# Performance work log

Hardware: AMD Instinct MI355X
Metric: run time of the kernel (lower is better)

The kernel has to match this reference:

```python
import jax, jax.numpy as jnp
import numpy as np

B, S, E, H = 16, 2048, 128, 128  # batch, seq_len, n_embd, head_dim


def setup_inputs() -> dict:
    key = jax.random.key(0)
    ks = jax.random.split(key, 6)
    init_s = 1.0 / np.sqrt(E)  # ~ torch Linear default init scale
    return {
        "q": jax.random.normal(ks[0], (B, S, E), jnp.float32),
        "k": jax.random.normal(ks[1], (B, S, E), jnp.float32),
        "v": jax.random.normal(ks[2], (B, S, E), jnp.float32),
        "Wq": jax.random.normal(ks[3], (H, E), jnp.float32) * init_s,
        "bq": jnp.zeros((H,), jnp.float32),
        "Wk": jax.random.normal(ks[4], (H, E), jnp.float32) * init_s,
        "bk": jnp.zeros((H,), jnp.float32),
        "Wv": jax.random.normal(ks[5], (H, E), jnp.float32) * init_s,
        "bv": jnp.zeros((H,), jnp.float32),
        "mask": jnp.tril(jnp.ones((S, S), jnp.float32)),  # causal mask
    }


def reference(q, k, v, Wq, bq, Wk, bk, Wv, bv, mask):
    # Linear projections: y = x @ W.T + b (torch nn.Linear convention)
    qh = q @ Wq.T + bq  # [B,S,H]
    kh = k @ Wk.T + bk  # [B,S,H]
    vh = v @ Wv.T + bv  # [B,S,H]
    d_k = kh.shape[-1]
    wei = jnp.einsum("bqd,bkd->bqk", qh, kh) * (d_k ** -0.5)  # [B,S,S]
    wei = jnp.where(mask == 0, -jnp.inf, wei)  # masked_fill(mask==0, -inf)
    attn = jax.nn.softmax(wei, axis=-1)
    return jnp.einsum("bqk,bkd->bqd", attn, vh)  # [B,S,H]
```

## Files before the change

### kernel.cpp

```cpp
#include <hip/hip_runtime.h>
#include <hip/hip_bf16.h>

#define BATCH 16
#define SEQ   2048
#define HD    128
#define TB    64
#define QB3   64
#define KB3   64
#define NT3   (SEQ/QB3)
#define PLANE ((size_t)BATCH*SEQ*HD)

typedef __attribute__((ext_vector_type(8))) short bf16x8;
typedef __attribute__((ext_vector_type(4))) float f32x4;
typedef __attribute__((ext_vector_type(2))) unsigned int u32x2;

#define MFMA(a,b,c) __builtin_amdgcn_mfma_f32_16x16x32_bf16(a,b,c,0,0,0)

__device__ __forceinline__ short f2bf(float f){
  union{float f; unsigned u;} v; v.f = f;
  unsigned r = (v.u + 0x7FFFu + ((v.u>>16)&1u))>>16;
  return (short)r;
}
__device__ __forceinline__ unsigned packbf(float lo, float hi){
  return ((unsigned)(unsigned short)f2bf(hi) << 16) | (unsigned short)f2bf(lo);
}
__device__ __forceinline__ bf16x8 pack8(f32x4 a, f32x4 b){
  bf16x8 r;
  r[0]=f2bf(a[0]); r[1]=f2bf(a[1]); r[2]=f2bf(a[2]); r[3]=f2bf(a[3]);
  r[4]=f2bf(b[0]); r[5]=f2bf(b[1]); r[6]=f2bf(b[2]); r[7]=f2bf(b[3]);
  return r;
}
__device__ __forceinline__ bf16x8 ldfrag(const float* base, size_t eo){
  const float* p = base + eo;
  return pack8(*(const f32x4*)p, *(const f32x4*)(p+4));
}

__global__ __launch_bounds__(256)
void wconv_kernel(const float* __restrict__ Wq, const float* __restrict__ Wk,
                  const float* __restrict__ Wv, short* __restrict__ wb)
{
  int i = (blockIdx.x*256 + threadIdx.x)*8;
  const float* src = (i < 16384) ? Wq : (i < 32768 ? Wk : Wv);
  int off = i & 16383;
  f32x4 a = *(const f32x4*)(src + off);
  f32x4 b = *(const f32x4*)(src + off + 4);
  *(bf16x8*)(wb + i) = pack8(a, b);
}

__global__ __launch_bounds__(256)
void proj_kernel(const float* __restrict__ q, const float* __restrict__ k,
                 const float* __restrict__ v,
                 const float* __restrict__ bq, const float* __restrict__ bk,
                 const float* __restrict__ bv,
                 const short* __restrict__ wb, short* __restrict__ ws)
{
  __shared__ __align__(16) short T[TB*136];
  __shared__ __align__(16) short VT[HD*72];

  const int z = blockIdx.y;
  const float* x  = z==0 ? q  : (z==1 ? k  : v);
  const float* bb = z==0 ? bq : (z==1 ? bk : bv);
  const short* W  = wb + (size_t)z*HD*HD;

  const int tid = threadIdx.x;
  const int w = tid>>6, l = tid&63, li = l&15, g = l>>4;
  const int bx = blockIdx.x;
  const int rowbase = bx*TB + w*16;

  bf16x8 afr[4];
  const float* xr = x + (size_t)(rowbase+li)*HD + g*8;
  #pragma unroll
  for (int ks=0; ks<4; ks++) afr[ks] = ldfrag(xr, (size_t)ks*32);

  f32x4 acc[8];
  #pragma unroll
  for (int ct=0; ct<8; ct++) acc[ct] = (f32x4){0.f,0.f,0.f,0.f};
  #pragma unroll
  for (int ct=0; ct<8; ct++){
    #pragma unroll
    for (int ks=0; ks<4; ks++){
      bf16x8 bfr = *(const bf16x8*)(W + (size_t)(ct*16+li)*HD + ks*32 + g*8);
      acc[ct] = MFMA(afr[ks], bfr, acc[ct]);
    }
  }

  const int img  = (bx>>1);
  const int half = bx & 1;

  if (z < 2){
    #pragma unroll
    for (int ct=0; ct<8; ct++){
      float bias = bb[ct*16+li];
      #pragma unroll
      for (int r=0; r<4; r++)
        T[(w*16+g*4+r)*136 + ct*16+li] = f2bf(acc[ct][r] + bias);
    }
    __syncthreads();
    if (z == 0){
      short* dst = ws + (size_t)bx*TB*HD;
      #pragma unroll
      for (int it=0; it<4; it++){
        int c = tid + it*256, row = c>>4, c8 = c&15;
        *(bf16x8*)(dst + row*HD + c8*8) = *(const bf16x8*)&T[row*136 + c8*8];
      }
    } else {
      short* dst = ws + PLANE + (size_t)img*16384;
      #pragma unroll
      for (int it=0; it<4; it++){
        int c = tid + it*256, row = c>>4, c8 = c&15;
        int r128 = half*64 + row;
        int chunk = r128*16 + (c8 ^ (r128&7));
        *(bf16x8*)(dst + chunk*8) = *(const bf16x8*)&T[row*136 + c8*8];
      }
    }
  } else {
    #pragma unroll
    for (int ct=0; ct<8; ct++){
      float bias = bb[ct*16+li];
      #pragma unroll
      for (int r=0; r<4; r++)
        VT[(ct*16+li)*72 + w*16+g*4+r] = f2bf(acc[ct][r] + bias);
    }
    __syncthreads();
    short* dst = ws + 2*PLANE + (size_t)img*16384;
    const int d = tid>>1, hf = tid&1;
    #pragma unroll
    for (int j=0; j<4; j++){
      int c8l = hf*4 + j;
      int c8g = half*8 + c8l;
      int chunk = d*16 + (c8g ^ (d&7));
      *(bf16x8*)(dst + chunk*8) = *(const bf16x8*)&VT[d*72 + c8l*8];
    }
  }
}

__global__ __launch_bounds__(256, 2)
void attn_kernel(const short* __restrict__ ws, float* __restrict__ out)
{
  __shared__ __align__(16) short KVL[2][16384];
  __shared__ __align__(16) short PL[4][16*72];

  const int bid  = blockIdx.x;
  const int xcd  = bid & 7, slot = bid >> 3;
  const int b    = xcd*2 + (slot >> 5);
  const int sl   = slot & 31;
  const int qt   = (slot < 32) ? sl : (31 - sl);

  const int tid = threadIdx.x;
  const int w = tid>>6, l = tid&63, li = l&15, g = l>>4;

  const short* Qw    = ws;
  const short* KimgB = ws + PLANE   + (size_t)b*(SEQ/128)*16384;
  const short* VimgB = ws + 2*PLANE + (size_t)b*(SEQ/128)*16384;

  const size_t qbase = (size_t)b*SEQ + qt*QB3;
  short* Pw = &PL[w][0];
  const float sc = 0.088388347648318447f;

  bf16x8 qfr[4];
  #pragma unroll
  for (int ks=0; ks<4; ks++)
    qfr[ks] = *(const bf16x8*)&Qw[(qbase + w*16 + li)*HD + ks*32 + g*8];

  f32x4 oacc[8];
  #pragma unroll
  for (int dt=0; dt<8; dt++) oacc[dt] = (f32x4){0.f,0.f,0.f,0.f};
  float mreg = -1e30f, lreg = 0.f;

  bf16x8 stg[8];
  #define LOADT(kt_) do{                                                     \
    const short* sK = KimgB + (size_t)((kt_)>>1)*16384 + ((kt_)&1)*8192;     \
    const short* sV = VimgB + (size_t)((kt_)>>1)*16384;                      \
    const int vh = ((kt_)&1)*8;                                              \
    _Pragma("unroll")                                                        \
    for (int j=0;j<4;j++) stg[j] = *(const bf16x8*)(sK + (tid + j*256)*8);   \
    _Pragma("unroll")                                                        \
    for (int j=0;j<4;j++){                                                   \
      int i = tid + j*256, d = i>>3, c8s = i&7;                              \
      stg[4+j] = *(const bf16x8*)(sV + (d*16 + vh + c8s)*8);                 \
    }                                                                        \
  }while(0)
  #define WRT(nb_) do{                                                      \
    short* dK = &KVL[nb_][0];                                               \
    short* dV = &KVL[nb_][8192];                                            \
    _Pragma("unroll")                                                       \
    for (int j=0;j<4;j++) *(bf16x8*)(dK + (tid+j*256)*8) = stg[j];          \
    _Pragma("unroll")                                                       \
    for (int j=0;j<4;j++) *(bf16x8*)(dV + (tid+j*256)*8) = stg[4+j];        \
  }while(0)

  LOADT(0); WRT(0); __syncthreads();
  int cur = 0;

  for (int kt=0; kt<=qt; kt++){
    const bool pre = (kt < qt);
    if (pre) LOADT(kt+1);

    const short* KL = &KVL[cur][0];
    const short* VL = &KVL[cur][8192];

    f32x4 st[4];
    #pragma unroll
    for (int ct=0; ct<4; ct++) st[ct] = (f32x4){0.f,0.f,0.f,0.f};
    __builtin_amdgcn_s_setprio(1);
    #pragma unroll
    for (int ct=0; ct<4; ct++){
      const int row = ct*16 + li;
      #pragma unroll
      for (int ks=0; ks<4; ks++){
        const int chunk = row*16 + ((ks*4 + g) ^ (row&7));
        bf16x8 kfr = *(const bf16x8*)&KL[chunk*8];
        st[ct] = MFMA(kfr, qfr[ks], st[ct]);
      }
    }
    __builtin_amdgcn_s_setprio(0);

    float sv[4][4];
    float pm = -1e30f;
    const bool diag = (kt == qt);
    const int qloc = w*16 + li;
    #pragma unroll
    for (int ct=0; ct<4; ct++){
      #pragma unroll
      for (int r=0; r<4; r++){
        float x = st[ct][r]*sc;
        if (diag && (ct*16 + g*4 + r) > qloc) x = -1e30f;
        sv[ct][r] = x;
        pm = fmaxf(pm, x);
      }
    }
    pm = fmaxf(pm, __shfl_xor(pm, 16));
    pm = fmaxf(pm, __shfl_xor(pm, 32));
    float mn   = fmaxf(mreg, pm);
    float sclq = __expf(mreg - mn);
    mreg = mn;
    float psum = 0.f;
    #pragma unroll
    for (int ct=0; ct<4; ct++){
      #pragma unroll
      for (int r=0; r<4; r++){
        float p = __expf(sv[ct][r] - mn);
        sv[ct][r] = p;
        psum += p;
      }
    }
    psum += __shfl_xor(psum, 16);
    psum += __shfl_xor(psum, 32);
    lreg = lreg*sclq + psum;

    float sclo[4];
    #pragma unroll
    for (int r=0; r<4; r++) sclo[r] = __shfl(sclq, g*4 + r);
    #pragma unroll
    for (int dt=0; dt<8; dt++){
      #pragma unroll
      for (int r=0; r<4; r++) oacc[dt][r] *= sclo[r];
    }

    #pragma unroll
    for (int c4=0; c4<4; c4++){
      u32x2 pw;
      pw[0] = packbf(sv[c4][0], sv[c4][1]);
      pw[1] = packbf(sv[c4][2], sv[c4][3]);
      *(u32x2*)&Pw[li*72 + c4*16 + g*4] = pw;
    }
    __builtin_amdgcn_s_setprio(1);
    #pragma unroll
    for (int ks2=0; ks2<2; ks2++){
      bf16x8 afr = *(const bf16x8*)&Pw[li*72 + ks2*32 + g*8];
      #pragma unroll
      for (int dt=0; dt<8; dt++){
        const int d = dt*16 + li;
        const int chunk = d*8 + ((ks2*4 + g) ^ (d&7));
        bf16x8 bfr = *(const bf16x8*)&VL[chunk*8];
        oacc[dt] = MFMA(afr, bfr, oacc[dt]);
      }
    }
    __builtin_amdgcn_s_setprio(0);

    if (pre) WRT(cur^1);
    __syncthreads();
    cur ^= 1;
  }

  float lso[4];
  #pragma unroll
  for (int r=0; r<4; r++) lso[r] = __shfl(lreg, g*4 + r);
  float* Ob = out + qbase*HD;
  #pragma unroll
  for (int dt=0; dt<8; dt++){
    #pragma unroll
    for (int r=0; r<4; r++){
      Ob[(size_t)(w*16 + g*4 + r)*HD + dt*16 + li] = oacc[dt][r] / lso[r];
    }
  }
  #undef LOADT
  #undef WRT
}

extern "C" void kernel_launch(void* const* d_in, const int* in_sizes, int n_in,
                              void* d_out, int out_size, void* d_ws, size_t ws_size,
                              hipStream_t stream)
{
  short* ws = (short*)d_ws;
  short* wb = ws + 3*PLANE;

  wconv_kernel<<<24, 256, 0, stream>>>(
      (const float*)d_in[3], (const float*)d_in[5], (const float*)d_in[7], wb);

  dim3 pg(BATCH*SEQ/TB, 3);
  proj_kernel<<<pg, 256, 0, stream>>>(
      (const float*)d_in[0], (const float*)d_in[1], (const float*)d_in[2],
      (const float*)d_in[4], (const float*)d_in[6], (const float*)d_in[8],
      wb, ws);

  attn_kernel<<<dim3(BATCH*NT3), 256, 0, stream>>>(ws, (float*)d_out);
}
```

Before: 99.43 us.

## Fuse Q projection into attention kernel prologue

Removes the Q branch from the projection kernel and computes Q = x·Wqᵀ + bq inside the attention kernel, using MFMA on fp32 inputs converted to bf16. The result is staged through the K/V shared buffer to get the A-fragment layout. This avoids writing the projected Q plane to workspace and reading it back, and shrinks the projection grid by a third. In exchange, attention blocks pay extra prologue work and two more barriers before the main loop, overlapped with the first K/V tile load.

```diff
diff --git a/kernel.cpp b/kernel.cpp
--- a/kernel.cpp
+++ b/kernel.cpp
@@ -6,7 +6,6 @@
 #define HD    128
 #define TB    64
 #define QB3   64
-#define KB3   64
 #define NT3   (SEQ/QB3)
 #define PLANE ((size_t)BATCH*SEQ*HD)
 
@@ -48,18 +47,16 @@
 }
 
 __global__ __launch_bounds__(256)
-void proj_kernel(const float* __restrict__ q, const float* __restrict__ k,
-                 const float* __restrict__ v,
-                 const float* __restrict__ bq, const float* __restrict__ bk,
-                 const float* __restrict__ bv,
+void proj_kernel(const float* __restrict__ k, const float* __restrict__ v,
+                 const float* __restrict__ bk, const float* __restrict__ bv,
                  const short* __restrict__ wb, short* __restrict__ ws)
 {
   __shared__ __align__(16) short T[TB*136];
   __shared__ __align__(16) short VT[HD*72];
 
-  const int z = blockIdx.y;
-  const float* x  = z==0 ? q  : (z==1 ? k  : v);
-  const float* bb = z==0 ? bq : (z==1 ? bk : bv);
+  const int z = blockIdx.y + 1;
+  const float* x  = (z==1) ? k  : v;
+  const float* bb = (z==1) ? bk : bv;
   const short* W  = wb + (size_t)z*HD*HD;
 
   const int tid = threadIdx.x;
@@ -87,7 +84,7 @@
   const int img  = (bx>>1);
   const int half = bx & 1;
 
-  if (z < 2){
+  if (z == 1){
     #pragma unroll
     for (int ct=0; ct<8; ct++){
       float bias = bb[ct*16+li];
@@ -96,22 +93,13 @@
         T[(w*16+g*4+r)*136 + ct*16+li] = f2bf(acc[ct][r] + bias);
     }
     __syncthreads();
-    if (z == 0){
-      short* dst = ws + (size_t)bx*TB*HD;
-      #pragma unroll
-      for (int it=0; it<4; it++){
-        int c = tid + it*256, row = c>>4, c8 = c&15;
-        *(bf16x8*)(dst + row*HD + c8*8) = *(const bf16x8*)&T[row*136 + c8*8];
-      }
-    } else {
-      short* dst = ws + PLANE + (size_t)img*16384;
-      #pragma unroll
-      for (int it=0; it<4; it++){
-        int c = tid + it*256, row = c>>4, c8 = c&15;
-        int r128 = half*64 + row;
-        int chunk = r128*16 + (c8 ^ (r128&7));
-        *(bf16x8*)(dst + chunk*8) = *(const bf16x8*)&T[row*136 + c8*8];
-      }
+    short* dst = ws + PLANE + (size_t)img*16384;
+    #pragma unroll
+    for (int it=0; it<4; it++){
+      int c = tid + it*256, row = c>>4, c8 = c&15;
+      int r128 = half*64 + row;
+      int chunk = r128*16 + (c8 ^ (r128&7));
+      *(bf16x8*)(dst + chunk*8) = *(const bf16x8*)&T[row*136 + c8*8];
     }
   } else {
     #pragma unroll
@@ -135,7 +123,9 @@
 }
 
 __global__ __launch_bounds__(256, 2)
-void attn_kernel(const short* __restrict__ ws, float* __restrict__ out)
+void attn_kernel(const float* __restrict__ qin, const float* __restrict__ bq,
+                 const short* __restrict__ wb, const short* __restrict__ ws,
+                 float* __restrict__ out)
 {
   __shared__ __align__(16) short KVL[2][16384];
   __shared__ __align__(16) short PL[4][16*72];
@@ -149,23 +139,12 @@
   const int tid = threadIdx.x;
   const int w = tid>>6, l = tid&63, li = l&15, g = l>>4;
 
-  const short* Qw    = ws;
   const short* KimgB = ws + PLANE   + (size_t)b*(SEQ/128)*16384;
   const short* VimgB = ws + 2*PLANE + (size_t)b*(SEQ/128)*16384;
 
   const size_t qbase = (size_t)b*SEQ + qt*QB3;
   short* Pw = &PL[w][0];
   const float sc = 0.088388347648318447f;
-
-  bf16x8 qfr[4];
-  #pragma unroll
-  for (int ks=0; ks<4; ks++)
-    qfr[ks] = *(const bf16x8*)&Qw[(qbase + w*16 + li)*HD + ks*32 + g*8];
-
-  f32x4 oacc[8];
-  #pragma unroll
-  for (int dt=0; dt<8; dt++) oacc[dt] = (f32x4){0.f,0.f,0.f,0.f};
-  float mreg = -1e30f, lreg = 0.f;
 
   bf16x8 stg[8];
   #define LOADT(kt_) do{                                                     \
@@ -189,7 +168,46 @@
     for (int j=0;j<4;j++) *(bf16x8*)(dV + (tid+j*256)*8) = stg[4+j];        \
   }while(0)
 
-  LOADT(0); WRT(0); __syncthreads();
+  LOADT(0);
+
+  bf16x8 qfr[4];
+  {
+    bf16x8 xa[4];
+    const float* xr = qin + (qbase + w*16 + li)*HD + g*8;
+    #pragma unroll
+    for (int ks=0; ks<4; ks++) xa[ks] = ldfrag(xr, (size_t)ks*32);
+    f32x4 qa[8];
+    #pragma unroll
+    for (int ct=0; ct<8; ct++) qa[ct] = (f32x4){0.f,0.f,0.f,0.f};
+    #pragma unroll
+    for (int ct=0; ct<8; ct++){
+      #pragma unroll
+      for (int ks=0; ks<4; ks++){
+        bf16x8 wf = *(const bf16x8*)(wb + (size_t)(ct*16+li)*HD + ks*32 + g*8);
+        qa[ct] = MFMA(xa[ks], wf, qa[ct]);
+      }
+    }
+    short* T = &KVL[0][0];
+    #pragma unroll
+    for (int ct=0; ct<8; ct++){
+      float bias = bq[ct*16+li];
+      #pragma unroll
+      for (int r=0; r<4; r++)
+        T[(w*16+g*4+r)*136 + ct*16+li] = f2bf(qa[ct][r] + bias);
+    }
+    __syncthreads();
+    #pragma unroll
+    for (int ks=0; ks<4; ks++)
+      qfr[ks] = *(const bf16x8*)&T[(w*16+li)*136 + ks*32 + g*8];
+    __syncthreads();
+  }
+
+  f32x4 oacc[8];
+  #pragma unroll
+  for (int dt=0; dt<8; dt++) oacc[dt] = (f32x4){0.f,0.f,0.f,0.f};
+  float mreg = -1e30f, lreg = 0.f;
+
+  WRT(0); __syncthreads();
   int cur = 0;
 
   for (int kt=0; kt<=qt; kt++){
@@ -308,11 +326,12 @@
   wconv_kernel<<<24, 256, 0, stream>>>(
       (const float*)d_in[3], (const float*)d_in[5], (const float*)d_in[7], wb);
 
-  dim3 pg(BATCH*SEQ/TB, 3);
+  dim3 pg(BATCH*SEQ/TB, 2);
   proj_kernel<<<pg, 256, 0, stream>>>(
-      (const float*)d_in[0], (const float*)d_in[1], (const float*)d_in[2],
-      (const float*)d_in[4], (const float*)d_in[6], (const float*)d_in[8],
+      (const float*)d_in[1], (const float*)d_in[2],
+      (const float*)d_in[6], (const float*)d_in[8],
       wb, ws);
 
-  attn_kernel<<<dim3(BATCH*NT3), 256, 0, stream>>>(ws, (float*)d_out);
-}
+  attn_kernel<<<dim3(BATCH*NT3), 256, 0, stream>>>(
+      (const float*)d_in[0], (const float*)d_in[4], wb, ws, (float*)d_out);
+}
```

After: 96.24 us. -3.2%, faster.
